# Optimization experiments

Measured on AMD Instinct MI355X. Metric: run time of the kernel, lower is better.

Reference implementation:

```python
import jax, jax.numpy as jnp
import numpy as np

N_NODES = 50000   # total nodes across the batch of graphs
N_EDGES = 800000  # avg degree 16
F_IN = 128        # num_features
DIM = 256         # hidden dim
N_LAYERS = 3      # num_gc_layers
N_GRAPHS = 512    # graphs in the batch (max(batch)+1)
BN_EPS = 1e-5


def setup_inputs() -> dict:
    key = jax.random.key(0)
    ks = jax.random.split(key, 16)
    inp = {}
    inp["x"] = jax.random.normal(ks[0], (N_NODES, F_IN), dtype=jnp.float32)
    inp["edge_index"] = jax.random.randint(ks[1], (2, N_EDGES), 0, N_NODES, dtype=jnp.int64)
    inp["batch"] = jnp.sort(jax.random.randint(ks[2], (N_NODES,), 0, N_GRAPHS, dtype=jnp.int64))
    k = 3
    for i in range(N_LAYERS):
        fin = F_IN if i == 0 else DIM
        inp[f"w1_{i}"] = jax.random.normal(ks[k], (fin, DIM), dtype=jnp.float32) / np.sqrt(fin); k += 1
        inp[f"b1_{i}"] = jnp.zeros((DIM,), dtype=jnp.float32)
        inp[f"w2_{i}"] = jax.random.normal(ks[k], (DIM, DIM), dtype=jnp.float32) / np.sqrt(DIM); k += 1
        inp[f"b2_{i}"] = jnp.zeros((DIM,), dtype=jnp.float32)
        inp[f"bn_g{i}"] = jnp.ones((DIM,), dtype=jnp.float32)
        inp[f"bn_b{i}"] = jnp.zeros((DIM,), dtype=jnp.float32)
    return inp


def _gin_layer(h, src, dst, w1, b1, w2, b2, g, b):
    # GINConv (eps=0): agg_i = h_i + sum_{j->i} h_j  (scatter-add over edges)
    agg = h + jax.ops.segment_sum(h[src], dst, num_segments=N_NODES)
    # MLP: Linear -> ReLU -> Linear
    m = jnp.maximum(agg @ w1 + b1, 0.0) @ w2 + b2
    # F.relu then BatchNorm1d (training mode: batch statistics, biased var)
    m = jnp.maximum(m, 0.0)
    mu = m.mean(axis=0)
    var = ((m - mu) ** 2).mean(axis=0)
    return g * (m - mu) / jnp.sqrt(var + BN_EPS) + b


def reference(x, edge_index, batch,
              w1_0, b1_0, w2_0, b2_0, bn_g0, bn_b0,
              w1_1, b1_1, w2_1, b2_1, bn_g1, bn_b1,
              w1_2, b1_2, w2_2, b2_2, bn_g2, bn_b2):
    src, dst = edge_index[0], edge_index[1]
    params = [
        (w1_0, b1_0, w2_0, b2_0, bn_g0, bn_b0),
        (w1_1, b1_1, w2_1, b2_1, bn_g1, bn_b1),
        (w1_2, b1_2, w2_2, b2_2, bn_g2, bn_b2),
    ]
    xs = []
    h = x
    for p in params:
        h = _gin_layer(h, src, dst, *p)
        xs.append(h)
    # global add-pool readout per layer, concat along feature dim
    pooled = jnp.concatenate(
        [jax.ops.segment_sum(hi, batch, num_segments=N_GRAPHS) for hi in xs], axis=1)
    return pooled, jnp.concatenate(xs, axis=1)
```

## Files before the change

### kernel.cpp

```cpp
#include <hip/hip_runtime.h>

#define N_NODES 50000
#define N_EDGES 800000
#define F_IN 128
#define DIM 256
#define N_GRAPHS 512
#define BN_EPS 1e-5f

typedef unsigned short u16;
typedef unsigned int u32;
using floatx4 = __attribute__((ext_vector_type(4))) float;
using short8 = __attribute__((ext_vector_type(8))) short;
using half2v = __attribute__((ext_vector_type(2))) _Float16;

#if __has_builtin(__builtin_amdgcn_fdot2)
#define HAS_FDOT2 1
#endif

__device__ __forceinline__ u16 f2h(float f) {
    _Float16 h = (_Float16)f;
    return __builtin_bit_cast(u16, h);
}
__device__ __forceinline__ float hlo(u32 u) {
    half2v h = __builtin_bit_cast(half2v, u);
    return (float)h.x;
}
__device__ __forceinline__ float hhi(u32 u) {
    half2v h = __builtin_bit_cast(half2v, u);
    return (float)h.y;
}
__device__ __forceinline__ u32 pack2(float a, float b) {
    half2v h = {(_Float16)a, (_Float16)b};
    return __builtin_bit_cast(u32, h);
}
__device__ __forceinline__ void dacc(u32 w, float& a, float& b) {
#ifdef HAS_FDOT2
    half2v v = __builtin_bit_cast(half2v, w);
    const half2v L = {(_Float16)1.0f, (_Float16)0.0f};
    const half2v Hm = {(_Float16)0.0f, (_Float16)1.0f};
    a = __builtin_amdgcn_fdot2(v, L, a, false);
    b = __builtin_amdgcn_fdot2(v, Hm, b, false);
#else
    a += hlo(w);
    b += hhi(w);
#endif
}
__device__ __forceinline__ void load_lds16(const void* g, void* l) {
    __builtin_amdgcn_global_load_lds((const __attribute__((address_space(1))) void*)g,
                                     (__attribute__((address_space(3))) void*)l, 16, 0, 0);
}


__global__ void count_deg(const int* __restrict__ dst, int* __restrict__ deg, int nE) {
    int e = blockIdx.x * 256 + threadIdx.x;
    if (e < nE) atomicAdd(&deg[dst[e]], 1);
}

__global__ void scan_block(const int* __restrict__ deg, int* __restrict__ row_start,
                           int* __restrict__ bsum, int n) {
    __shared__ int wtot[4];
    int i = blockIdx.x * 256 + threadIdx.x;
    int lane = threadIdx.x & 63, w = threadIdx.x >> 6;
    int v = (i < n) ? deg[i] : 0;
    int s = v;
#pragma unroll
    for (int d = 1; d < 64; d <<= 1) {
        int t = __shfl_up(s, d);
        if (lane >= d) s += t;
    }
    if (lane == 63) wtot[w] = s;
    __syncthreads();
    int off = 0;
#pragma unroll
    for (int k = 0; k < 4; ++k)
        if (k < w) off += wtot[k];
    s += off;
    if (i < n) row_start[i + 1] = s;
    if (threadIdx.x == 255) bsum[blockIdx.x] = s;
}

__global__ void scan_partials(const int* __restrict__ bsum, int* __restrict__ boff,
                              int* __restrict__ row_start, int* __restrict__ cursor, int nb) {
    __shared__ int wtot[4];
    int i = threadIdx.x;
    int lane = i & 63, w = i >> 6;
    int v = (i < nb) ? bsum[i] : 0;
    int s = v;
#pragma unroll
    for (int d = 1; d < 64; d <<= 1) {
        int t = __shfl_up(s, d);
        if (lane >= d) s += t;
    }
    if (lane == 63) wtot[w] = s;
    __syncthreads();
    int off = 0;
#pragma unroll
    for (int k = 0; k < 4; ++k)
        if (k < w) off += wtot[k];
    boff[i] = s + off - v;
    if (i == 0) { row_start[0] = 0; cursor[0] = 0; }
}

__global__ void add_offsets(int* __restrict__ row_start, int* __restrict__ cursor,
                            const int* __restrict__ boff, int n) {
    int i = blockIdx.x * 256 + threadIdx.x;
    if (i < n) {
        int fin = row_start[i + 1] + boff[blockIdx.x];
        row_start[i + 1] = fin;
        cursor[i + 1] = fin;
    }
}

__global__ void fill_csr(const int* __restrict__ src, const int* __restrict__ dst,
                         int* __restrict__ cursor, int* __restrict__ srcs, int nE) {
    int e = blockIdx.x * 256 + threadIdx.x;
    if (e < nE) {
        int p = atomicAdd(&cursor[dst[e]], 1);
        srcs[p] = src[e];
    }
}


__global__ void convert_all(const float4* __restrict__ x4, uint2* __restrict__ Hout, int n4,
                            const float* __restrict__ w10, const float* __restrict__ w11,
                            const float* __restrict__ w12, const float* __restrict__ w20,
                            const float* __restrict__ w21, const float* __restrict__ w22,
                            u16* __restrict__ Wall) {
    int i = blockIdx.x * 256 + threadIdx.x;
    if (i < n4) {
        float4 v = x4[i];
        uint2 p;
        p.x = pack2(v.x, v.y);
        p.y = pack2(v.z, v.w);
        Hout[i] = p;
        return;
    }
    int j = i - n4;
    if (j >= 360448) return;
    const float* w;
    int K, base;
    if (j < 32768)       { w = w10; K = 128; base = 0; }
    else if (j < 98304)  { w = w11; K = 256; base = 32768; }
    else if (j < 163840) { w = w12; K = 256; base = 98304; }
    else if (j < 229376) { w = w20; K = 256; base = 163840; }
    else if (j < 294912) { w = w21; K = 256; base = 229376; }
    else                 { w = w22; K = 256; base = 294912; }
    int loc = j - base;
    int nn = loc / K, kk = loc - nn * K;
    Wall[j] = f2h(w[(size_t)kk * 256 + nn]);
}


template <int K>
__global__ __launch_bounds__(256) void aggregate_v2(
    const u16* __restrict__ h, const int* __restrict__ row_start,
    const int* __restrict__ srcs, u16* __restrict__ outp, int n) {
    constexpr int RW = K / 2;
    constexpr int NSUB = (K == 256) ? 2 : 4;
    int node = (int)(((size_t)blockIdx.x * blockDim.x + threadIdx.x) >> 6);
    int lane = threadIdx.x & 63;
    if (node >= n) return;
    const u32* hb = (const u32*)h;
    const int sub = lane / (64 / NSUB);
    const int li = lane % (64 / NSUB);

    float acc[8];
#pragma unroll
    for (int t = 0; t < 8; ++t) acc[t] = 0.f;
    {
        if (sub == 0) {
            uint4 v = *(const uint4*)(hb + (size_t)node * RW + li * 4);
            dacc(v.x, acc[0], acc[1]);
            dacc(v.y, acc[2], acc[3]);
            dacc(v.z, acc[4], acc[5]);
            dacc(v.w, acc[6], acc[7]);
        }
    }

    int s = row_start[node], e = row_start[node + 1];
    for (int j0 = s; j0 < e; j0 += 64) {
        int myidx = (j0 + lane < e) ? srcs[j0 + lane] : 0;
        int cnt = min(64, e - j0);
        int j = 0;
        for (; j + NSUB * 8 - 1 < cnt; j += NSUB * 8) {
            uint4 g[8];
#pragma unroll
            for (int q = 0; q < 8; ++q) {
                int sq = __shfl(myidx, j + q * NSUB + sub);
                g[q] = *(const uint4*)(hb + (size_t)sq * RW + li * 4);
            }
#pragma unroll
            for (int q = 0; q < 8; ++q) {
                dacc(g[q].x, acc[0], acc[1]);
                dacc(g[q].y, acc[2], acc[3]);
                dacc(g[q].z, acc[4], acc[5]);
                dacc(g[q].w, acc[6], acc[7]);
            }
        }
        for (; j + NSUB * 4 - 1 < cnt; j += NSUB * 4) {
            uint4 g[4];
#pragma unroll
            for (int q = 0; q < 4; ++q) {
                int sq = __shfl(myidx, j + q * NSUB + sub);
                g[q] = *(const uint4*)(hb + (size_t)sq * RW + li * 4);
            }
#pragma unroll
            for (int q = 0; q < 4; ++q) {
                dacc(g[q].x, acc[0], acc[1]);
                dacc(g[q].y, acc[2], acc[3]);
                dacc(g[q].z, acc[4], acc[5]);
                dacc(g[q].w, acc[6], acc[7]);
            }
        }
        for (; j < cnt; j += NSUB) {
            int idx = j + sub;
            bool valid = idx < cnt;
            int sq = __shfl(myidx, valid ? idx : j);
            if (valid) {
                uint4 g = *(const uint4*)(hb + (size_t)sq * RW + li * 4);
                dacc(g.x, acc[0], acc[1]);
                dacc(g.y, acc[2], acc[3]);
                dacc(g.z, acc[4], acc[5]);
                dacc(g.w, acc[6], acc[7]);
            }
        }
    }

    if (NSUB == 4) {
#pragma unroll
        for (int t = 0; t < 8; ++t) acc[t] += __shfl_xor(acc[t], 16);
    }
#pragma unroll
    for (int t = 0; t < 8; ++t) acc[t] += __shfl_xor(acc[t], 32);

    if (sub == 0) {
        uint4 o;
        o.x = pack2(acc[0], acc[1]);
        o.y = pack2(acc[2], acc[3]);
        o.z = pack2(acc[4], acc[5]);
        o.w = pack2(acc[6], acc[7]);
        *(uint4*)((u32*)outp + (size_t)node * RW + li * 4) = o;
    }
}


template <int MODE>
__global__ __launch_bounds__(512) void gemm_mfma(
    const u16* __restrict__ A, const u16* __restrict__ Bt, const float* __restrict__ bias,
    u16* __restrict__ Cout, float* __restrict__ sums, int M, int K) {
    __shared__ u16 As[128 * 32];
    __shared__ u16 Bs[256 * 32];
    const int tid = threadIdx.x;
    const int w = tid >> 6, lane = tid & 63;
    const int wm = w >> 2, wn = w & 3;
    const int r = lane & 15, rg = lane >> 4;
    const int bm = blockIdx.x * 128;

    floatx4 acc[4][4];
#pragma unroll
    for (int i = 0; i < 4; ++i)
#pragma unroll
        for (int j = 0; j < 4; ++j) acc[i][j] = (floatx4){0.f, 0.f, 0.f, 0.f};

    for (int k0 = 0; k0 < K; k0 += 32) {
        __syncthreads();
        {
            int arow = bm + (tid >> 2);
            if (arow >= M) arow = M - 1;
            load_lds16(A + (size_t)arow * K + k0 + (tid & 3) * 8, As + w * 512);
#pragma unroll
            for (int q = 0; q < 2; ++q) {
                int i = q * 512 + tid;
                int nrow = i >> 2;
                load_lds16(Bt + (size_t)nrow * K + k0 + (i & 3) * 8, Bs + (q * 8 + w) * 512);
            }
        }
        __syncthreads();
        short8 a[4], b[4];
#pragma unroll
        for (int mi = 0; mi < 4; ++mi)
            a[mi] = *(const short8*)(As + (wm * 64 + mi * 16 + r) * 32 + rg * 8);
#pragma unroll
        for (int ni = 0; ni < 4; ++ni)
            b[ni] = *(const short8*)(Bs + (wn * 64 + ni * 16 + r) * 32 + rg * 8);
#pragma unroll
        for (int mi = 0; mi < 4; ++mi)
#pragma unroll
            for (int ni = 0; ni < 4; ++ni)
                acc[mi][ni] = __builtin_amdgcn_mfma_f32_16x16x32_f16(a[mi], b[ni], acc[mi][ni], 0, 0, 0);
    }

    if (MODE == 0) {
#pragma unroll
        for (int ni = 0; ni < 4; ++ni) {
            int col = wn * 64 + ni * 16 + r;
            float bv = bias[col];
#pragma unroll
            for (int mi = 0; mi < 4; ++mi)
#pragma unroll
                for (int rr = 0; rr < 4; ++rr) {
                    int row = bm + wm * 64 + mi * 16 + rg * 4 + rr;
                    if (row < M) Cout[(size_t)row * 256 + col] = f2h(fmaxf(acc[mi][ni][rr] + bv, 0.f));
                }
        }
    } else {
#pragma unroll
        for (int ni = 0; ni < 4; ++ni) {
            int col = wn * 64 + ni * 16 + r;
            float bv = bias[col];
            float s = 0.f, s2 = 0.f;
#pragma unroll
            for (int mi = 0; mi < 4; ++mi)
#pragma unroll
                for (int rr = 0; rr < 4; ++rr) {
                    int row = bm + wm * 64 + mi * 16 + rg * 4 + rr;
                    if (row < M) {
                        float v = fmaxf(acc[mi][ni][rr] + bv, 0.f);
                        u16 qb = f2h(v);
                        float vq = hlo((u32)qb);
                        Cout[(size_t)row * 256 + col] = qb;
                        s += vq;
                        s2 += vq * vq;
                    }
                }
            s += __shfl_xor(s, 16);
            s += __shfl_xor(s, 32);
            s2 += __shfl_xor(s2, 16);
            s2 += __shfl_xor(s2, 32);
            if (rg == 0) {
                atomicAdd(&sums[col], s);
                atomicAdd(&sums[256 + col], s2);
            }
        }
    }
}


template <int WRITE_H>
__global__ void bn_apply_pool(const u16* __restrict__ Mb, const float* __restrict__ sums,
                              const float* __restrict__ g, const float* __restrict__ bb,
                              const int* __restrict__ batch, float* __restrict__ out_nodes,
                              u16* __restrict__ H, float* __restrict__ pooled,
                              int col_off, int n, float inv_n) {
    int w = threadIdx.x >> 6, lane = threadIdx.x & 63;
    int base = blockIdx.x * 64 + w * 16;
    if (base >= n) return;
    int c4 = lane << 2;
    float4 s1 = *(const float4*)(sums + c4);
    float4 s2 = *(const float4*)(sums + 256 + c4);
    float4 g4 = *(const float4*)(g + c4);
    float4 b4 = *(const float4*)(bb + c4);
    float4 sc, sh;
    {
        float mux = s1.x * inv_n, muy = s1.y * inv_n, muz = s1.z * inv_n, muw = s1.w * inv_n;
        sc.x = g4.x / sqrtf(s2.x * inv_n - mux * mux + BN_EPS);
        sc.y = g4.y / sqrtf(s2.y * inv_n - muy * muy + BN_EPS);
        sc.z = g4.z / sqrtf(s2.z * inv_n - muz * muz + BN_EPS);
        sc.w = g4.w / sqrtf(s2.w * inv_n - muw * muw + BN_EPS);
        sh.x = b4.x - mux * sc.x;
        sh.y = b4.y - muy * sc.y;
        sh.z = b4.z - muz * sc.z;
        sh.w = b4.w - muw * sc.w;
    }
    float4 acc = make_float4(0.f, 0.f, 0.f, 0.f);
    int gcur = -1;
    int end = min(base + 16, n);
    for (int row = base; row < end; ++row) {
        uint2 pk = *(const uint2*)(Mb + (size_t)row * 256 + c4);
        float4 o;
        o.x = fmaf(hlo(pk.x), sc.x, sh.x);
        o.y = fmaf(hhi(pk.x), sc.y, sh.y);
        o.z = fmaf(hlo(pk.y), sc.z, sh.z);
        o.w = fmaf(hhi(pk.y), sc.w, sh.w);
        floatx4 ov = {o.x, o.y, o.z, o.w};
        __builtin_nontemporal_store(ov, (floatx4*)(out_nodes + (size_t)row * 768 + col_off + c4));
        if (WRITE_H) {
            uint2 hk;
            hk.x = pack2(o.x, o.y);
            hk.y = pack2(o.z, o.w);
            *(uint2*)(H + (size_t)row * 256 + c4) = hk;
        }
        int gg = batch[row];
        if (gg != gcur) {
            if (gcur >= 0) {
                float* pp = pooled + (size_t)gcur * 768 + col_off + c4;
                atomicAdd(pp + 0, acc.x);
                atomicAdd(pp + 1, acc.y);
                atomicAdd(pp + 2, acc.z);
                atomicAdd(pp + 3, acc.w);
            }
            gcur = gg;
            acc = o;
        } else {
            acc.x += o.x; acc.y += o.y; acc.z += o.z; acc.w += o.w;
        }
    }
    if (gcur >= 0) {
        float* pp = pooled + (size_t)gcur * 768 + col_off + c4;
        atomicAdd(pp + 0, acc.x);
        atomicAdd(pp + 1, acc.y);
        atomicAdd(pp + 2, acc.z);
        atomicAdd(pp + 3, acc.w);
    }
}


extern "C" void kernel_launch(void* const* d_in, const int* in_sizes, int n_in,
                              void* d_out, int out_size, void* d_ws, size_t ws_size,
                              hipStream_t stream) {
    const float* x = (const float*)d_in[0];
    const int* esrc = (const int*)d_in[1];
    const int* edst = esrc + N_EDGES;
    const int* batch = (const int*)d_in[2];

    const float* w1[3] = {(const float*)d_in[3], (const float*)d_in[9], (const float*)d_in[15]};
    const float* b1[3] = {(const float*)d_in[4], (const float*)d_in[10], (const float*)d_in[16]};
    const float* w2[3] = {(const float*)d_in[5], (const float*)d_in[11], (const float*)d_in[17]};
    const float* b2[3] = {(const float*)d_in[6], (const float*)d_in[12], (const float*)d_in[18]};
    const float* bng[3] = {(const float*)d_in[7], (const float*)d_in[13], (const float*)d_in[19]};
    const float* bnb[3] = {(const float*)d_in[8], (const float*)d_in[14], (const float*)d_in[20]};

    float* out_pooled = (float*)d_out;
    float* out_nodes = (float*)d_out + (size_t)N_GRAPHS * 768;

    char* p = (char*)d_ws;
    u16* Abf = (u16*)p; p += (size_t)N_NODES * 256 * 2;
    u16* T = (u16*)p;   p += (size_t)N_NODES * 256 * 2;
    u16* H = (u16*)p;   p += (size_t)N_NODES * 256 * 2;
    u16* Wall = (u16*)p; p += (size_t)360448 * 2;
    float* sums = (float*)p; p += 3 * 512 * 4;
    int* deg = (int*)p;      p += (size_t)N_NODES * 4;
    const size_t zero_bytes = 3 * 512 * 4 + (size_t)N_NODES * 4;
    int* row_start = (int*)p; p += (size_t)(N_NODES + 1) * 4;
    int* cursor = (int*)p;    p += (size_t)(N_NODES + 1) * 4;
    int* srcs = (int*)p;      p += (size_t)N_EDGES * 4;
    int* bsum = (int*)p;      p += 256 * 4;
    int* boff = (int*)p;      p += 256 * 4;

    const u16* W1t[3] = {Wall, Wall + 32768, Wall + 98304};
    const u16* W2t[3] = {Wall + 163840, Wall + 229376, Wall + 294912};

    const int NBLK = (N_NODES + 255) / 256;

    hipMemsetAsync(sums, 0, zero_bytes, stream);
    hipMemsetAsync(out_pooled, 0, (size_t)N_GRAPHS * 768 * sizeof(float), stream);

    count_deg<<<(N_EDGES + 255) / 256, 256, 0, stream>>>(edst, deg, N_EDGES);
    scan_block<<<NBLK, 256, 0, stream>>>(deg, row_start, bsum, N_NODES);
    scan_partials<<<1, 256, 0, stream>>>(bsum, boff, row_start, cursor, NBLK);
    add_offsets<<<NBLK, 256, 0, stream>>>(row_start, cursor, boff, N_NODES);
    fill_csr<<<(N_EDGES + 255) / 256, 256, 0, stream>>>(esrc, edst, cursor, srcs, N_EDGES);

    {
        const int n4 = N_NODES * F_IN / 4;
        const int tot = n4 + 360448;
        convert_all<<<(tot + 255) / 256, 256, 0, stream>>>(
            (const float4*)x, (uint2*)H, n4,
            w1[0], w1[1], w1[2], w2[0], w2[1], w2[2], Wall);
    }

    const int AGRID = (N_NODES + 3) / 4;
    const int GGRID = (N_NODES + 127) / 128;
    const int PBLK = (N_NODES + 63) / 64;
    for (int L = 0; L < 3; ++L) {
        int K1 = (L == 0) ? F_IN : DIM;
        float* sumsL = sums + L * 512;
        if (L == 0)
            aggregate_v2<128><<<AGRID, 256, 0, stream>>>(H, row_start, srcs, Abf, N_NODES);
        else
            aggregate_v2<256><<<AGRID, 256, 0, stream>>>(H, row_start, srcs, Abf, N_NODES);
        gemm_mfma<0><<<GGRID, 512, 0, stream>>>(Abf, W1t[L], b1[L], T, nullptr, N_NODES, K1);
        gemm_mfma<1><<<GGRID, 512, 0, stream>>>(T, W2t[L], b2[L], Abf, sumsL, N_NODES, DIM);
        if (L < 2)
            bn_apply_pool<1><<<PBLK, 256, 0, stream>>>(Abf, sumsL, bng[L], bnb[L], batch,
                                                       out_nodes, H, out_pooled, L * 256, N_NODES, 1.0f / N_NODES);
        else
            bn_apply_pool<0><<<PBLK, 256, 0, stream>>>(Abf, sumsL, bng[L], bnb[L], batch,
                                                       out_nodes, H, out_pooled, L * 256, N_NODES, 1.0f / N_NODES);
    }
}
```

Before: 702.4 us.

## Fuse the two MLP GEMMs into one kernel, keeping the hidden tile in LDS

```diff
diff --git a/kernel.cpp b/kernel.cpp
--- a/kernel.cpp
+++ b/kernel.cpp
@@ -244,93 +244,120 @@
 }
 
 
-template <int MODE>
-__global__ __launch_bounds__(512) void gemm_mfma(
-    const u16* __restrict__ A, const u16* __restrict__ Bt, const float* __restrict__ bias,
-    u16* __restrict__ Cout, float* __restrict__ sums, int M, int K) {
-    __shared__ u16 As[128 * 32];
+template <int K1>
+__global__ __launch_bounds__(512, 4) void mlp_fused(
+    const u16* __restrict__ A, const u16* __restrict__ B1t, const float* __restrict__ b1,
+    const u16* __restrict__ B2t, const float* __restrict__ b2,
+    u16* __restrict__ Cout, float* __restrict__ sums, int M) {
+    __shared__ u16 As[64 * 32];
     __shared__ u16 Bs[256 * 32];
+    __shared__ u16 Ts[64 * 256];
     const int tid = threadIdx.x;
     const int w = tid >> 6, lane = tid & 63;
     const int wm = w >> 2, wn = w & 3;
     const int r = lane & 15, rg = lane >> 4;
-    const int bm = blockIdx.x * 128;
-
-    floatx4 acc[4][4];
-#pragma unroll
-    for (int i = 0; i < 4; ++i)
+    const int bm = blockIdx.x * 64;
+
+    floatx4 acc[2][4];
+#pragma unroll
+    for (int i = 0; i < 2; ++i)
 #pragma unroll
         for (int j = 0; j < 4; ++j) acc[i][j] = (floatx4){0.f, 0.f, 0.f, 0.f};
 
-    for (int k0 = 0; k0 < K; k0 += 32) {
+    for (int k0 = 0; k0 < K1; k0 += 32) {
         __syncthreads();
-        {
+        if (tid < 256) {
             int arow = bm + (tid >> 2);
             if (arow >= M) arow = M - 1;
-            load_lds16(A + (size_t)arow * K + k0 + (tid & 3) * 8, As + w * 512);
-#pragma unroll
-            for (int q = 0; q < 2; ++q) {
-                int i = q * 512 + tid;
-                int nrow = i >> 2;
-                load_lds16(Bt + (size_t)nrow * K + k0 + (i & 3) * 8, Bs + (q * 8 + w) * 512);
-            }
+            load_lds16(A + (size_t)arow * K1 + k0 + (tid & 3) * 8, As + w * 512);
+        }
+#pragma unroll
+        for (int q = 0; q < 2; ++q) {
+            int i = q * 512 + tid;
+            load_lds16(B1t + (size_t)(i >> 2) * K1 + k0 + (i & 3) * 8, Bs + (q * 8 + w) * 512);
         }
         __syncthreads();
-        short8 a[4], b[4];
-#pragma unroll
-        for (int mi = 0; mi < 4; ++mi)
-            a[mi] = *(const short8*)(As + (wm * 64 + mi * 16 + r) * 32 + rg * 8);
+        short8 a[2], b[4];
+#pragma unroll
+        for (int mi = 0; mi < 2; ++mi)
+            a[mi] = *(const short8*)(As + (wm * 32 + mi * 16 + r) * 32 + rg * 8);
 #pragma unroll
         for (int ni = 0; ni < 4; ++ni)
             b[ni] = *(const short8*)(Bs + (wn * 64 + ni * 16 + r) * 32 + rg * 8);
 #pragma unroll
-        for (int mi = 0; mi < 4; ++mi)
+        for (int mi = 0; mi < 2; ++mi)
 #pragma unroll
             for (int ni = 0; ni < 4; ++ni)
                 acc[mi][ni] = __builtin_amdgcn_mfma_f32_16x16x32_f16(a[mi], b[ni], acc[mi][ni], 0, 0, 0);
     }
-
-    if (MODE == 0) {
-#pragma unroll
-        for (int ni = 0; ni < 4; ++ni) {
-            int col = wn * 64 + ni * 16 + r;
-            float bv = bias[col];
-#pragma unroll
-            for (int mi = 0; mi < 4; ++mi)
-#pragma unroll
-                for (int rr = 0; rr < 4; ++rr) {
-                    int row = bm + wm * 64 + mi * 16 + rg * 4 + rr;
-                    if (row < M) Cout[(size_t)row * 256 + col] = f2h(fmaxf(acc[mi][ni][rr] + bv, 0.f));
+#pragma unroll
+    for (int ni = 0; ni < 4; ++ni) {
+        int col = wn * 64 + ni * 16 + r;
+        float bv = b1[col];
+#pragma unroll
+        for (int mi = 0; mi < 2; ++mi)
+#pragma unroll
+            for (int rr = 0; rr < 4; ++rr) {
+                int lrow = wm * 32 + mi * 16 + rg * 4 + rr;
+                float v = fmaxf(acc[mi][ni][rr] + bv, 0.f);
+                int chunk = (col >> 3) ^ (lrow & 7);
+                *(u16*)((char*)Ts + lrow * 512 + chunk * 16 + (col & 7) * 2) = f2h(v);
+            }
+#pragma unroll
+        for (int mi = 0; mi < 2; ++mi) acc[mi][ni] = (floatx4){0.f, 0.f, 0.f, 0.f};
+    }
+
+    for (int k0 = 0; k0 < 256; k0 += 32) {
+        __syncthreads();
+#pragma unroll
+        for (int q = 0; q < 2; ++q) {
+            int i = q * 512 + tid;
+            load_lds16(B2t + (size_t)(i >> 2) * 256 + k0 + (i & 3) * 8, Bs + (q * 8 + w) * 512);
+        }
+        __syncthreads();
+        short8 a[2], b[4];
+#pragma unroll
+        for (int mi = 0; mi < 2; ++mi) {
+            int lrow = wm * 32 + mi * 16 + r;
+            int chunk = ((k0 >> 3) + rg) ^ (lrow & 7);
+            a[mi] = *(const short8*)((const char*)Ts + lrow * 512 + chunk * 16);
+        }
+#pragma unroll
+        for (int ni = 0; ni < 4; ++ni)
+            b[ni] = *(const short8*)(Bs + (wn * 64 + ni * 16 + r) * 32 + rg * 8);
+#pragma unroll
+        for (int mi = 0; mi < 2; ++mi)
+#pragma unroll
+            for (int ni = 0; ni < 4; ++ni)
+                acc[mi][ni] = __builtin_amdgcn_mfma_f32_16x16x32_f16(a[mi], b[ni], acc[mi][ni], 0, 0, 0);
+    }
+
+#pragma unroll
+    for (int ni = 0; ni < 4; ++ni) {
+        int col = wn * 64 + ni * 16 + r;
+        float bv = b2[col];
+        float s = 0.f, s2 = 0.f;
+#pragma unroll
+        for (int mi = 0; mi < 2; ++mi)
+#pragma unroll
+            for (int rr = 0; rr < 4; ++rr) {
+                int row = bm + wm * 32 + mi * 16 + rg * 4 + rr;
+                if (row < M) {
+                    float v = fmaxf(acc[mi][ni][rr] + bv, 0.f);
+                    u16 qb = f2h(v);
+                    float vq = hlo((u32)qb);
+                    Cout[(size_t)row * 256 + col] = qb;
+                    s += vq;
+                    s2 += vq * vq;
                 }
-        }
-    } else {
-#pragma unroll
-        for (int ni = 0; ni < 4; ++ni) {
-            int col = wn * 64 + ni * 16 + r;
-            float bv = bias[col];
-            float s = 0.f, s2 = 0.f;
-#pragma unroll
-            for (int mi = 0; mi < 4; ++mi)
-#pragma unroll
-                for (int rr = 0; rr < 4; ++rr) {
-                    int row = bm + wm * 64 + mi * 16 + rg * 4 + rr;
-                    if (row < M) {
-                        float v = fmaxf(acc[mi][ni][rr] + bv, 0.f);
-                        u16 qb = f2h(v);
-                        float vq = hlo((u32)qb);
-                        Cout[(size_t)row * 256 + col] = qb;
-                        s += vq;
-                        s2 += vq * vq;
-                    }
-                }
-            s += __shfl_xor(s, 16);
-            s += __shfl_xor(s, 32);
-            s2 += __shfl_xor(s2, 16);
-            s2 += __shfl_xor(s2, 32);
-            if (rg == 0) {
-                atomicAdd(&sums[col], s);
-                atomicAdd(&sums[256 + col], s2);
-            }
+            }
+        s += __shfl_xor(s, 16);
+        s += __shfl_xor(s, 32);
+        s2 += __shfl_xor(s2, 16);
+        s2 += __shfl_xor(s2, 32);
+        if (rg == 0) {
+            atomicAdd(&sums[col], s);
+            atomicAdd(&sums[256 + col], s2);
         }
     }
 }
@@ -425,7 +452,7 @@
 
     char* p = (char*)d_ws;
     u16* Abf = (u16*)p; p += (size_t)N_NODES * 256 * 2;
-    u16* T = (u16*)p;   p += (size_t)N_NODES * 256 * 2;
+    u16* Mb = (u16*)p;  p += (size_t)N_NODES * 256 * 2;
     u16* H = (u16*)p;   p += (size_t)N_NODES * 256 * 2;
     u16* Wall = (u16*)p; p += (size_t)360448 * 2;
     float* sums = (float*)p; p += 3 * 512 * 4;
@@ -460,22 +487,24 @@
     }
 
     const int AGRID = (N_NODES + 3) / 4;
-    const int GGRID = (N_NODES + 127) / 128;
+    const int MGRID = (N_NODES + 63) / 64;
     const int PBLK = (N_NODES + 63) / 64;
     for (int L = 0; L < 3; ++L) {
-        int K1 = (L == 0) ? F_IN : DIM;
         float* sumsL = sums + L * 512;
-        if (L == 0)
+        if (L == 0) {
             aggregate_v2<128><<<AGRID, 256, 0, stream>>>(H, row_start, srcs, Abf, N_NODES);
-        else
+            mlp_fused<128><<<MGRID, 512, 0, stream>>>(Abf, W1t[L], b1[L], W2t[L], b2[L],
+                                                      Mb, sumsL, N_NODES);
+        } else {
             aggregate_v2<256><<<AGRID, 256, 0, stream>>>(H, row_start, srcs, Abf, N_NODES);
-        gemm_mfma<0><<<GGRID, 512, 0, stream>>>(Abf, W1t[L], b1[L], T, nullptr, N_NODES, K1);
-        gemm_mfma<1><<<GGRID, 512, 0, stream>>>(T, W2t[L], b2[L], Abf, sumsL, N_NODES, DIM);
+            mlp_fused<256><<<MGRID, 512, 0, stream>>>(Abf, W1t[L], b1[L], W2t[L], b2[L],
+                                                      Mb, sumsL, N_NODES);
+        }
         if (L < 2)
-            bn_apply_pool<1><<<PBLK, 256, 0, stream>>>(Abf, sumsL, bng[L], bnb[L], batch,
+            bn_apply_pool<1><<<PBLK, 256, 0, stream>>>(Mb, sumsL, bng[L], bnb[L], batch,
                                                        out_nodes, H, out_pooled, L * 256, N_NODES, 1.0f / N_NODES);
         else
-            bn_apply_pool<0><<<PBLK, 256, 0, stream>>>(Abf, sumsL, bng[L], bnb[L], batch,
+            bn_apply_pool<0><<<PBLK, 256, 0, stream>>>(Mb, sumsL, bng[L], bnb[L], batch,
                                                        out_nodes, H, out_pooled, L * 256, N_NODES, 1.0f / N_NODES);
     }
 }
```

Result: no change. 703.2 us (+0.1%).
